# Optimization experiments

Measured on AMD Instinct MI355X. Metric: run time of the kernel, lower is better.

Reference implementation:

```python
import jax, jax.numpy as jnp
import numpy as np

EPS = 1e-12


def sage_pool_conv(x, src, dst, W_pool, b_pool, W_self, W_neigh, b, num_nodes):
    """DGL SAGEConv with aggregator_type='pool':
    h_neigh[v] = max_{u in N(v)} relu(x[u] @ W_pool + b_pool)
    out[v] = x[v] @ W_self + h_neigh[v] @ W_neigh + b
    Zero-in-degree nodes get h_neigh = 0 (DGL fills max over empty set with 0).
    """
    m = jax.nn.relu(x[src] @ W_pool + b_pool)            # [E, F] gathered + transformed
    agg = jax.ops.segment_max(m, dst, num_segments=num_nodes)  # [N, F], -inf where no neighbors
    agg = jnp.where(jnp.isneginf(agg), 0.0, agg)
    return x @ W_self + agg @ W_neigh + b


def l2norm_relu(h):
    # F.normalize(h, p=2, dim=1, eps=1e-12) then relu
    n = jnp.maximum(jnp.linalg.norm(h, axis=1, keepdims=True), EPS)
    return jax.nn.relu(h / n)


def setup_inputs() -> dict:
    key = jax.random.key(0)
    N, E = 50000, 1600000
    IN, HID, OUT = 128, 128, 128
    ks = jax.random.split(key, 16)
    s = 0.05
    return {
        "x": jax.random.normal(ks[0], (N, IN), dtype=jnp.float32),
        "src": jax.random.randint(ks[1], (E,), 0, N, dtype=jnp.int32),
        "dst": jax.random.randint(ks[2], (E,), 0, N, dtype=jnp.int32),
        "W_pool1": jax.random.normal(ks[3], (IN, IN), dtype=jnp.float32) * s,
        "b_pool1": jnp.zeros((IN,), dtype=jnp.float32),
        "W_self1": jax.random.normal(ks[4], (IN, HID), dtype=jnp.float32) * s,
        "W_neigh1": jax.random.normal(ks[5], (IN, HID), dtype=jnp.float32) * s,
        "b1": jnp.zeros((HID,), dtype=jnp.float32),
        "W_pool2": jax.random.normal(ks[6], (HID, HID), dtype=jnp.float32) * s,
        "b_pool2": jnp.zeros((HID,), dtype=jnp.float32),
        "W_self2": jax.random.normal(ks[7], (HID, OUT), dtype=jnp.float32) * s,
        "W_neigh2": jax.random.normal(ks[8], (HID, OUT), dtype=jnp.float32) * s,
        "b2": jnp.zeros((OUT,), dtype=jnp.float32),
    }


def reference(x, src, dst, W_pool1, b_pool1, W_self1, W_neigh1, b1,
              W_pool2, b_pool2, W_self2, W_neigh2, b2):
    N = x.shape[0]
    h = sage_pool_conv(x, src, dst, W_pool1, b_pool1, W_self1, W_neigh1, b1, N)
    h = l2norm_relu(h)
    # dropout_1 is re-assigned in the original forward but never applied -> no dropout
    h = sage_pool_conv(h, src, dst, W_pool2, b_pool2, W_self2, W_neigh2, b2, N)
    h = l2norm_relu(h)
    return h
```

## Files before the change

### kernel.cpp

```cpp
#include <hip/hip_runtime.h>
#include <hip/hip_bf16.h>

#define NF 128

typedef __attribute__((ext_vector_type(8))) short bf8;
typedef __attribute__((ext_vector_type(4))) float f4;
typedef unsigned short u16x8 __attribute__((ext_vector_type(8)));

static __device__ __forceinline__ unsigned short f2bf(float f) {
  unsigned u = __builtin_bit_cast(unsigned, f);
  u = u + 0x7FFF + ((u >> 16) & 1);
  return (unsigned short)(u >> 16);
}

static __device__ __forceinline__ uint4 pkmax4(uint4 a, uint4 b) {
  u16x8 x = __builtin_bit_cast(u16x8, a);
  u16x8 y = __builtin_bit_cast(u16x8, b);
  u16x8 m = __builtin_elementwise_max(x, y);
  return __builtin_bit_cast(uint4, m);
}

static __device__ __forceinline__ uint4 shflxor4(uint4 a, int m) {
  uint4 r;
  r.x = (unsigned)__shfl_xor((int)a.x, m, 64);
  r.y = (unsigned)__shfl_xor((int)a.y, m, 64);
  r.z = (unsigned)__shfl_xor((int)a.z, m, 64);
  r.w = (unsigned)__shfl_xor((int)a.w, m, 64);
  return r;
}


#define TILE_B 8192

__global__ __launch_bounds__(256) void k_prep(
    const float* __restrict__ x, unsigned short* __restrict__ Xb, long long nelX,
    const int* __restrict__ dst, int* __restrict__ bcnt, int E, int gTile,
    const float* W0, const float* W1, const float* W2,
    const float* W3, const float* W4, const float* W5,
    unsigned short* __restrict__ Wpack) {
  __shared__ int h[256];
  int b = blockIdx.x, tid = threadIdx.x;

  long long i = ((long long)b * 256 + tid) * 8;
  if (i + 8 <= nelX) {
    float4 a = *(const float4*)(x + i);
    float4 c = *(const float4*)(x + i + 4);
    uint4 o;
    o.x = f2bf(a.x) | ((unsigned)f2bf(a.y) << 16);
    o.y = f2bf(a.z) | ((unsigned)f2bf(a.w) << 16);
    o.z = f2bf(c.x) | ((unsigned)f2bf(c.y) << 16);
    o.w = f2bf(c.z) | ((unsigned)f2bf(c.w) << 16);
    *(uint4*)(Xb + i) = o;
  }

  if (b < gTile) {
    h[tid] = 0;
    __syncthreads();
    int t0 = b * TILE_B;
    int tend = min(E, t0 + TILE_B);
    for (int k = t0 + tid; k < tend; k += 256) atomicAdd(&h[dst[k] >> 8], 1);
    __syncthreads();
    if (h[tid] > 0) atomicAdd(&bcnt[tid], h[tid]);
  } else if (b < gTile + 48) {
    int gid = (b - gTile) * 256 + tid;
    int m = gid >> 11;
    int u = gid & 2047;
    const float* W = (m == 0) ? W0 : (m == 1) ? W1 : (m == 2) ? W2
                   : (m == 3) ? W3 : (m == 4) ? W4 : W5;
    int l = u & 63, c = u >> 6;
    int kk = c & 3, t = c >> 2;
    int kb = kk * 32 + ((l >> 4) << 3);
    int n = t * 16 + (l & 15);
    unsigned short* o = Wpack + (size_t)m * 2048 * 8 + (size_t)u * 8;
    #pragma unroll
    for (int j = 0; j < 8; ++j) o[j] = f2bf(W[(size_t)(kb + j) * NF + n]);
  }
}


__global__ __launch_bounds__(256) void k_bscan(const int* __restrict__ bcnt,
                                               int* __restrict__ boff,
                                               int* __restrict__ cursors,
                                               int* __restrict__ off,
                                               int nb, int N, int E) {
  __shared__ int sc[256];
  int tid = threadIdx.x;
  int v = (tid < nb) ? bcnt[tid] : 0;
  sc[tid] = v;
  __syncthreads();
  for (int d = 1; d < 256; d <<= 1) {
    int t = (tid >= d) ? sc[tid - d] : 0;
    __syncthreads();
    sc[tid] += t;
    __syncthreads();
  }
  if (tid < nb) {
    boff[tid + 1] = sc[tid];
    cursors[tid] = sc[tid] - v;
  }
  if (tid == 0) { boff[0] = 0; off[N] = E; }
}

__global__ __launch_bounds__(256) void k_binB(const int* __restrict__ src,
                                              const int* __restrict__ dst,
                                              int* __restrict__ cursors,
                                              unsigned* __restrict__ tmp, int E) {
  __shared__ int h[256], sc[256], gb[256], lc[256];
  __shared__ unsigned sorted[TILE_B];
  int tid = threadIdx.x;
  int t0 = blockIdx.x * TILE_B;
  int tcnt = min(E - t0, TILE_B);
  if (tcnt <= 0) return;
  h[tid] = 0;
  __syncthreads();
  for (int i = tid; i < tcnt; i += 256) atomicAdd(&h[dst[t0 + i] >> 8], 1);
  __syncthreads();
  int v = h[tid];
  sc[tid] = v;
  __syncthreads();
  for (int d = 1; d < 256; d <<= 1) {
    int t = (tid >= d) ? sc[tid - d] : 0;
    __syncthreads();
    sc[tid] += t;
    __syncthreads();
  }
  lc[tid] = 0;
  gb[tid] = (v > 0) ? atomicAdd(&cursors[tid], v) : 0;
  __syncthreads();
  for (int i = tid; i < tcnt; i += 256) {
    int d = dst[t0 + i];
    unsigned s = (unsigned)src[t0 + i];
    int b = d >> 8;
    int p = (sc[b] - h[b]) + atomicAdd(&lc[b], 1);
    sorted[p] = ((unsigned)b << 24) | (s << 8) | (unsigned)(d & 255);
  }
  __syncthreads();
  for (int i = tid; i < tcnt; i += 256) {
    unsigned ev = sorted[i];
    int b = ev >> 24;
    tmp[gb[b] + (i - (sc[b] - h[b]))] = ev & 0xFFFFFFu;
  }
}

#define CSR_CAP 15360

__global__ __launch_bounds__(256) void k_binC(const unsigned* __restrict__ tmp,
                                              const int* __restrict__ boff,
                                              int* __restrict__ off,
                                              unsigned short* __restrict__ esrc, int N) {
  __shared__ int lh[256], ls[256], lcur[256];
  __shared__ int csr[CSR_CAP];
  int tid = threadIdx.x;
  int b = blockIdx.x;
  int base = b << 8;
  int beg = boff[b], end = boff[b + 1];
  int cnt = end - beg;
  lh[tid] = 0;
  __syncthreads();
  for (int i = beg + tid; i < end; i += 256) atomicAdd(&lh[tmp[i] & 255], 1);
  __syncthreads();
  int v = lh[tid];
  ls[tid] = v;
  __syncthreads();
  for (int d = 1; d < 256; d <<= 1) {
    int t = (tid >= d) ? ls[tid - d] : 0;
    __syncthreads();
    ls[tid] += t;
    __syncthreads();
  }
  int excl = ls[tid] - v;
  if (base + tid < N) off[base + tid] = beg + excl;
  lcur[tid] = 0;
  __syncthreads();
  if (cnt <= CSR_CAP) {
    for (int i = beg + tid; i < end; i += 256) {
      unsigned e = tmp[i];
      int dl = (int)(e & 255);
      int p = (ls[dl] - lh[dl]) + atomicAdd(&lcur[dl], 1);
      csr[p] = (int)(e >> 8);
    }
    __syncthreads();
    for (int i = tid; i < cnt; i += 256) esrc[beg + i] = (unsigned short)csr[i];
  } else {
    for (int i = beg + tid; i < end; i += 256) {
      unsigned e = tmp[i];
      int dl = (int)(e & 255);
      int p = (ls[dl] - lh[dl]) + atomicAdd(&lcur[dl], 1);
      esrc[beg + p] = (unsigned short)(e >> 8);
    }
  }
}


template <int NMAT, int OUT_MODE>
__global__ __launch_bounds__(512) void k_gemm_p(
    const unsigned short* __restrict__ A0, const unsigned short* __restrict__ P0,
    const unsigned short* __restrict__ A1, const unsigned short* __restrict__ P1,
    const float* __restrict__ bias, void* __restrict__ Cout, int M) {
  constexpr int STG = (OUT_MODE == 2) ? 8192 : 4096;
  __shared__ __align__(16) char smem[NMAT * 32768 + 8 * STG];
  int tid = threadIdx.x, w = tid >> 6, lane = tid & 63;
  int r0 = lane & 15, g = lane >> 4;

  {
    uint4* S = (uint4*)smem;
    const uint4* Pv0 = (const uint4*)P0;
    for (int t = tid; t < 2048; t += 512) S[t] = Pv0[t];
    if (NMAT == 2) {
      const uint4* Pv1 = (const uint4*)P1;
      for (int t = tid; t < 2048; t += 512) S[2048 + t] = Pv1[t];
    }
  }

  float bb[8];
  #pragma unroll
  for (int t = 0; t < 8; ++t) bb[t] = bias[t * 16 + r0];

  __syncthreads();
  const bf8* Wl = (const bf8*)smem;
  char* myst = smem + NMAT * 32768 + w * STG;

  int T = (M + 15) >> 4;
  int stride = gridDim.x * 8;
  for (int t0i = blockIdx.x * 8 + w; t0i < T; t0i += stride) {
    int rowbase = t0i * 16;
    int arow = min(rowbase + r0, M - 1);

    f4 acc[8];
    #pragma unroll
    for (int t = 0; t < 8; ++t) acc[t] = (f4){0.f, 0.f, 0.f, 0.f};

    #pragma unroll
    for (int mat = 0; mat < NMAT; ++mat) {
      const unsigned short* A = (mat == 0) ? A0 : A1;
      const bf8* Ar = (const bf8*)(A + (size_t)arow * NF);
      const bf8* Wm = Wl + mat * 2048;
      #pragma unroll
      for (int kk = 0; kk < 4; ++kk) {
        bf8 a = Ar[kk * 4 + g];
        #pragma unroll
        for (int t = 0; t < 8; ++t)
          acc[t] = __builtin_amdgcn_mfma_f32_16x16x32_bf16(a, Wm[(t * 4 + kk) * 64 + lane], acc[t], 0, 0, 0);
      }
    }

    float val[8][4];
    #pragma unroll
    for (int t = 0; t < 8; ++t)
      #pragma unroll
      for (int i = 0; i < 4; ++i) val[t][i] = acc[t][i] + bb[t];

    float inv[4] = {1.f, 1.f, 1.f, 1.f};
    if (OUT_MODE != 0) {
      float ss[4] = {0.f, 0.f, 0.f, 0.f};
      #pragma unroll
      for (int i = 0; i < 4; ++i)
        #pragma unroll
        for (int t = 0; t < 8; ++t) ss[i] += val[t][i] * val[t][i];
      #pragma unroll
      for (int d = 1; d < 16; d <<= 1)
        #pragma unroll
        for (int i = 0; i < 4; ++i) ss[i] += __shfl_xor(ss[i], d, 64);
      #pragma unroll
      for (int i = 0; i < 4; ++i) inv[i] = 1.f / fmaxf(sqrtf(ss[i]), 1e-12f);
    }

    int maxrows = min(16, M - rowbase);
    if (OUT_MODE == 2) {
      float* So = (float*)myst;
      #pragma unroll
      for (int i = 0; i < 4; ++i)
        #pragma unroll
        for (int t = 0; t < 8; ++t)
          So[(g * 4 + i) * NF + t * 16 + r0] = fmaxf(val[t][i] * inv[i], 0.f);
      uint4* Og = (uint4*)((float*)Cout + (size_t)rowbase * NF);
      const uint4* Sv = (const uint4*)myst;
      int maxc = maxrows * 32;
      #pragma unroll
      for (int k = 0; k < 8; ++k) {
        int c = lane + k * 64;
        if (c < maxc) Og[c] = Sv[c];
      }
    } else {
      unsigned short* So = (unsigned short*)myst;
      #pragma unroll
      for (int i = 0; i < 4; ++i)
        #pragma unroll
        for (int t = 0; t < 8; ++t)
          So[(g * 4 + i) * NF + t * 16 + r0] =
              f2bf(OUT_MODE == 0 ? fmaxf(val[t][i] + 0.f, 0.f) * 1.f
                                 : fmaxf(val[t][i] * inv[i], 0.f));
      uint4* Og = (uint4*)((unsigned short*)Cout + (size_t)rowbase * NF);
      const uint4* Sv = (const uint4*)myst;
      int maxc = maxrows * 16;
      #pragma unroll
      for (int k = 0; k < 4; ++k) {
        int c = lane + k * 64;
        if (c < maxc) Og[c] = Sv[c];
      }
    }
  }
}


__global__ __launch_bounds__(256) void k_gather_max(
    const unsigned short* __restrict__ Y, const int* __restrict__ off,
    const unsigned short* __restrict__ esrc, unsigned short* __restrict__ AGG, int N) {
  int w = (blockIdx.x * 256 + threadIdx.x) >> 6;
  int lane = threadIdx.x & 63;
  if (w >= N) return;
  int r0 = lane & 15, g = lane >> 4;
  int s = __builtin_amdgcn_readfirstlane(off[w]);
  int e = __builtin_amdgcn_readfirstlane(off[w + 1]);
  uint4 am[8];
  #pragma unroll
  for (int j = 0; j < 8; ++j) am[j] = (uint4){0u, 0u, 0u, 0u};
  for (int b0 = s; b0 < e; b0 += 64) {
    int cnt = min(64, e - b0);
    int idxv = (int)esrc[b0 + min(lane, cnt - 1)];
    for (int i = 0; i < cnt; i += 32) {
      uint4 v[8];
      #pragma unroll
      for (int j = 0; j < 8; ++j) {
        int eo = min(i + j * 4 + g, cnt - 1);
        int u = __shfl(idxv, eo, 64);
        v[j] = *((const uint4*)(Y + (size_t)u * NF) + r0);
      }
      #pragma unroll
      for (int j = 0; j < 8; ++j) am[j] = pkmax4(am[j], v[j]);
    }
  }
  am[0] = pkmax4(am[0], am[1]); am[2] = pkmax4(am[2], am[3]);
  am[4] = pkmax4(am[4], am[5]); am[6] = pkmax4(am[6], am[7]);
  am[0] = pkmax4(am[0], am[2]); am[4] = pkmax4(am[4], am[6]);
  uint4 a = pkmax4(am[0], am[4]);
  a = pkmax4(a, shflxor4(a, 16));
  a = pkmax4(a, shflxor4(a, 32));
  if (g == 0) *(uint4*)(AGG + (size_t)w * NF + r0 * 8) = a;
}


extern "C" void kernel_launch(void* const* d_in, const int* in_sizes, int n_in,
                              void* d_out, int out_size, void* d_ws, size_t ws_size,
                              hipStream_t stream) {
  const float* x   = (const float*)d_in[0];
  const int*   src = (const int*)d_in[1];
  const int*   dst = (const int*)d_in[2];
  const float* Wp1 = (const float*)d_in[3];
  const float* bp1 = (const float*)d_in[4];
  const float* Ws1 = (const float*)d_in[5];
  const float* Wn1 = (const float*)d_in[6];
  const float* b1  = (const float*)d_in[7];
  const float* Wp2 = (const float*)d_in[8];
  const float* bp2 = (const float*)d_in[9];
  const float* Ws2 = (const float*)d_in[10];
  const float* Wn2 = (const float*)d_in[11];
  const float* b2  = (const float*)d_in[12];
  float* out = (float*)d_out;

  const int N = in_sizes[0] / NF;
  const int E = in_sizes[1];
  const int NB = (N + 255) >> 8;

  char* ws = (char*)d_ws;
  auto carve = [&](size_t bytes) { char* p = ws; ws += (bytes + 255) & ~(size_t)255; return p; };
  unsigned short* Xb    = (unsigned short*)carve((size_t)N * NF * 2);
  unsigned short* Yb    = (unsigned short*)carve((size_t)N * NF * 2);
  unsigned short* AGGb  = (unsigned short*)carve((size_t)N * NF * 2);
  unsigned short* Hb    = (unsigned short*)carve((size_t)N * NF * 2);
  unsigned short* Wpack = (unsigned short*)carve((size_t)6 * NF * NF * 2);
  int* off     = (int*)carve((size_t)(N + 1) * 4);
  int* bcnt    = (int*)carve((size_t)NB * 4);
  int* boff    = (int*)carve((size_t)(NB + 1) * 4);
  int* cursors = (int*)carve((size_t)NB * 4);
  unsigned* tmp = (unsigned*)carve((size_t)E * 4);
  unsigned short* esrc = (unsigned short*)carve((size_t)E * 2);

  unsigned short* Pp1 = Wpack + 0 * NF * NF;
  unsigned short* Ps1 = Wpack + 1 * NF * NF;
  unsigned short* Pn1 = Wpack + 2 * NF * NF;
  unsigned short* Pp2 = Wpack + 3 * NF * NF;
  unsigned short* Ps2 = Wpack + 4 * NF * NF;
  unsigned short* Pn2 = Wpack + 5 * NF * NF;

  const long long nelX = (long long)N * NF;
  const int gConv = (int)((nelX / 8 + 255) / 256);
  const int gTile = (E + TILE_B - 1) / TILE_B;
  const int gRW   = (N + 3) / 4;

  hipMemsetAsync(bcnt, 0, (size_t)NB * 4, stream);
  k_prep<<<gConv, 256, 0, stream>>>(x, Xb, nelX, dst, bcnt, E, gTile,
                                    Wp1, Ws1, Wn1, Wp2, Ws2, Wn2, Wpack);
  k_bscan<<<1, 256, 0, stream>>>(bcnt, boff, cursors, off, NB, N, E);
  k_binB<<<gTile, 256, 0, stream>>>(src, dst, cursors, tmp, E);
  k_binC<<<NB, 256, 0, stream>>>(tmp, boff, off, esrc, N);

  k_gemm_p<1, 0><<<512, 512, 0, stream>>>(Xb, Pp1, nullptr, nullptr, bp1, Yb, N);
  k_gather_max<<<gRW, 256, 0, stream>>>(Yb, off, esrc, AGGb, N);
  k_gemm_p<2, 1><<<256, 512, 0, stream>>>(Xb, Ps1, AGGb, Pn1, b1, Hb, N);

  k_gemm_p<1, 0><<<512, 512, 0, stream>>>(Hb, Pp2, nullptr, nullptr, bp2, Yb, N);
  k_gather_max<<<gRW, 256, 0, stream>>>(Yb, off, esrc, AGGb, N);
  k_gemm_p<2, 2><<<256, 512, 0, stream>>>(Hb, Ps2, AGGb, Pn2, b2, out, N);
}
```

Before: 300.2 us.

## Drop bucket-scan kernel, slab-sort CSR by source, split GEMMs, shrink gather unroll

Removes the single-block k_bscan launch by having each k_binB and k_binC block recompute the bucket prefix sum from the counts. k_binC now sorts each node's edges into source-index slabs, so gathers within a node walk source rows roughly in ascending order for better cache locality. The dual GEMM becomes a one-tile-per-wave kernel that reads packed weights straight from global memory instead of staging them in LDS. The gather-max loop is reduced from 8 to 4 in-flight loads per lane. These trade redundant scans and less memory-level parallelism for one fewer launch, better locality and higher occupancy.

```diff
diff --git a/kernel.cpp b/kernel.cpp
--- a/kernel.cpp
+++ b/kernel.cpp
@@ -2,6 +2,10 @@
 #include <hip/hip_bf16.h>
 
 #define NF 128
+#define TILE_B 8192
+#define NSLAB 8
+#define SLAB_SHIFT 13
+#define CSR_CAP 15360
 
 typedef __attribute__((ext_vector_type(8))) short bf8;
 typedef __attribute__((ext_vector_type(4))) float f4;
@@ -29,8 +33,6 @@
   return r;
 }
 
-
-#define TILE_B 8192
 
 __global__ __launch_bounds__(256) void k_prep(
     const float* __restrict__ x, unsigned short* __restrict__ Xb, long long nelX,
@@ -78,105 +80,128 @@
 }
 
 
-__global__ __launch_bounds__(256) void k_bscan(const int* __restrict__ bcnt,
-                                               int* __restrict__ boff,
-                                               int* __restrict__ cursors,
-                                               int* __restrict__ off,
-                                               int nb, int N, int E) {
-  __shared__ int sc[256];
-  int tid = threadIdx.x;
-  int v = (tid < nb) ? bcnt[tid] : 0;
-  sc[tid] = v;
-  __syncthreads();
-  for (int d = 1; d < 256; d <<= 1) {
-    int t = (tid >= d) ? sc[tid - d] : 0;
-    __syncthreads();
-    sc[tid] += t;
-    __syncthreads();
-  }
-  if (tid < nb) {
-    boff[tid + 1] = sc[tid];
-    cursors[tid] = sc[tid] - v;
-  }
-  if (tid == 0) { boff[0] = 0; off[N] = E; }
-}
-
 __global__ __launch_bounds__(256) void k_binB(const int* __restrict__ src,
                                               const int* __restrict__ dst,
-                                              int* __restrict__ cursors,
+                                              const int* __restrict__ bcnt,
+                                              int* __restrict__ gcur,
                                               unsigned* __restrict__ tmp, int E) {
-  __shared__ int h[256], sc[256], gb[256], lc[256];
+  __shared__ int h[256], hs[256], gb[256], lc[256], bo[256];
   __shared__ unsigned sorted[TILE_B];
   int tid = threadIdx.x;
   int t0 = blockIdx.x * TILE_B;
   int tcnt = min(E - t0, TILE_B);
   if (tcnt <= 0) return;
+
+  int bv = bcnt[tid];
+  hs[tid] = bv;
+  __syncthreads();
+  for (int d = 1; d < 256; d <<= 1) {
+    int t = (tid >= d) ? hs[tid - d] : 0;
+    __syncthreads();
+    hs[tid] += t;
+    __syncthreads();
+  }
+  bo[tid] = hs[tid] - bv;
   h[tid] = 0;
   __syncthreads();
+
   for (int i = tid; i < tcnt; i += 256) atomicAdd(&h[dst[t0 + i] >> 8], 1);
   __syncthreads();
   int v = h[tid];
-  sc[tid] = v;
+  hs[tid] = v;
   __syncthreads();
   for (int d = 1; d < 256; d <<= 1) {
-    int t = (tid >= d) ? sc[tid - d] : 0;
-    __syncthreads();
-    sc[tid] += t;
+    int t = (tid >= d) ? hs[tid - d] : 0;
+    __syncthreads();
+    hs[tid] += t;
     __syncthreads();
   }
   lc[tid] = 0;
-  gb[tid] = (v > 0) ? atomicAdd(&cursors[tid], v) : 0;
+  gb[tid] = bo[tid] + ((v > 0) ? atomicAdd(&gcur[tid], v) : 0);
   __syncthreads();
   for (int i = tid; i < tcnt; i += 256) {
     int d = dst[t0 + i];
     unsigned s = (unsigned)src[t0 + i];
     int b = d >> 8;
-    int p = (sc[b] - h[b]) + atomicAdd(&lc[b], 1);
+    int p = (hs[b] - h[b]) + atomicAdd(&lc[b], 1);
     sorted[p] = ((unsigned)b << 24) | (s << 8) | (unsigned)(d & 255);
   }
   __syncthreads();
   for (int i = tid; i < tcnt; i += 256) {
     unsigned ev = sorted[i];
     int b = ev >> 24;
-    tmp[gb[b] + (i - (sc[b] - h[b]))] = ev & 0xFFFFFFu;
-  }
-}
-
-#define CSR_CAP 15360
+    tmp[gb[b] + (i - (hs[b] - h[b]))] = ev & 0xFFFFFFu;
+  }
+}
+
 
 __global__ __launch_bounds__(256) void k_binC(const unsigned* __restrict__ tmp,
-                                              const int* __restrict__ boff,
+                                              const int* __restrict__ bcnt,
                                               int* __restrict__ off,
-                                              unsigned short* __restrict__ esrc, int N) {
-  __shared__ int lh[256], ls[256], lcur[256];
+                                              unsigned short* __restrict__ esrc,
+                                              int N, int E) {
+  __shared__ int pre[256 * NSLAB];
+  __shared__ int lc2[256 * NSLAB];
+  __shared__ int s256[256];
+  __shared__ int bo[256];
   __shared__ int csr[CSR_CAP];
   int tid = threadIdx.x;
   int b = blockIdx.x;
   int base = b << 8;
-  int beg = boff[b], end = boff[b + 1];
-  int cnt = end - beg;
-  lh[tid] = 0;
-  __syncthreads();
-  for (int i = beg + tid; i < end; i += 256) atomicAdd(&lh[tmp[i] & 255], 1);
-  __syncthreads();
-  int v = lh[tid];
-  ls[tid] = v;
+
+  int bv = bcnt[tid];
+  s256[tid] = bv;
   __syncthreads();
   for (int d = 1; d < 256; d <<= 1) {
-    int t = (tid >= d) ? ls[tid - d] : 0;
-    __syncthreads();
-    ls[tid] += t;
-    __syncthreads();
-  }
-  int excl = ls[tid] - v;
-  if (base + tid < N) off[base + tid] = beg + excl;
-  lcur[tid] = 0;
-  __syncthreads();
+    int t = (tid >= d) ? s256[tid - d] : 0;
+    __syncthreads();
+    s256[tid] += t;
+    __syncthreads();
+  }
+  bo[tid] = s256[tid] - bv;
+  for (int k = tid; k < 256 * NSLAB; k += 256) { pre[k] = 0; lc2[k] = 0; }
+  __syncthreads();
+
+  int beg = bo[b];
+  int cnt = bcnt[b];
+  int end = beg + cnt;
+
+  for (int i = beg + tid; i < end; i += 256) {
+    unsigned e = tmp[i];
+    int key = ((e & 255) << 3) | (e >> (8 + SLAB_SHIFT));
+    atomicAdd(&pre[key], 1);
+  }
+  __syncthreads();
+  {
+    int sum = 0;
+    #pragma unroll
+    for (int j = 0; j < NSLAB; ++j) {
+      int v = pre[tid * NSLAB + j];
+      pre[tid * NSLAB + j] = sum;
+      sum += v;
+    }
+    s256[tid] = sum;
+    __syncthreads();
+    for (int d = 1; d < 256; d <<= 1) {
+      int t = (tid >= d) ? s256[tid - d] : 0;
+      __syncthreads();
+      s256[tid] += t;
+      __syncthreads();
+    }
+    int segbase = s256[tid] - sum;
+    #pragma unroll
+    for (int j = 0; j < NSLAB; ++j) pre[tid * NSLAB + j] += segbase;
+  }
+  __syncthreads();
+
+  if (base + tid < N) off[base + tid] = beg + pre[tid * NSLAB];
+  if (b == 0 && tid == 0) off[N] = E;
+
   if (cnt <= CSR_CAP) {
     for (int i = beg + tid; i < end; i += 256) {
       unsigned e = tmp[i];
-      int dl = (int)(e & 255);
-      int p = (ls[dl] - lh[dl]) + atomicAdd(&lcur[dl], 1);
+      int key = ((e & 255) << 3) | (e >> (8 + SLAB_SHIFT));
+      int p = pre[key] + atomicAdd(&lc2[key], 1);
       csr[p] = (int)(e >> 8);
     }
     __syncthreads();
@@ -184,41 +209,33 @@
   } else {
     for (int i = beg + tid; i < end; i += 256) {
       unsigned e = tmp[i];
-      int dl = (int)(e & 255);
-      int p = (ls[dl] - lh[dl]) + atomicAdd(&lcur[dl], 1);
+      int key = ((e & 255) << 3) | (e >> (8 + SLAB_SHIFT));
+      int p = pre[key] + atomicAdd(&lc2[key], 1);
       esrc[beg + p] = (unsigned short)(e >> 8);
     }
   }
 }
 
 
-template <int NMAT, int OUT_MODE>
-__global__ __launch_bounds__(512) void k_gemm_p(
-    const unsigned short* __restrict__ A0, const unsigned short* __restrict__ P0,
-    const unsigned short* __restrict__ A1, const unsigned short* __restrict__ P1,
-    const float* __restrict__ bias, void* __restrict__ Cout, int M) {
-  constexpr int STG = (OUT_MODE == 2) ? 8192 : 4096;
-  __shared__ __align__(16) char smem[NMAT * 32768 + 8 * STG];
+__global__ __launch_bounds__(512) void k_gemm_pool(
+    const unsigned short* __restrict__ A, const unsigned short* __restrict__ P,
+    const float* __restrict__ bias, unsigned short* __restrict__ Yout, int M) {
+  __shared__ __align__(16) char smem[32768 + 8 * 4096];
   int tid = threadIdx.x, w = tid >> 6, lane = tid & 63;
   int r0 = lane & 15, g = lane >> 4;
 
   {
     uint4* S = (uint4*)smem;
-    const uint4* Pv0 = (const uint4*)P0;
-    for (int t = tid; t < 2048; t += 512) S[t] = Pv0[t];
-    if (NMAT == 2) {
-      const uint4* Pv1 = (const uint4*)P1;
-      for (int t = tid; t < 2048; t += 512) S[2048 + t] = Pv1[t];
-    }
-  }
-
+    const uint4* Pv = (const uint4*)P;
+    for (int t = tid; t < 2048; t += 512) S[t] = Pv[t];
+  }
   float bb[8];
   #pragma unroll
   for (int t = 0; t < 8; ++t) bb[t] = bias[t * 16 + r0];
-
-  __syncthreads();
+  __syncthreads();
+
   const bf8* Wl = (const bf8*)smem;
-  char* myst = smem + NMAT * 32768 + w * STG;
+  char* myst = smem + 32768 + w * 4096;
 
   int T = (M + 15) >> 4;
   int stride = gridDim.x * 8;
@@ -230,74 +247,118 @@
     #pragma unroll
     for (int t = 0; t < 8; ++t) acc[t] = (f4){0.f, 0.f, 0.f, 0.f};
 
-    #pragma unroll
-    for (int mat = 0; mat < NMAT; ++mat) {
-      const unsigned short* A = (mat == 0) ? A0 : A1;
-      const bf8* Ar = (const bf8*)(A + (size_t)arow * NF);
-      const bf8* Wm = Wl + mat * 2048;
-      #pragma unroll
-      for (int kk = 0; kk < 4; ++kk) {
-        bf8 a = Ar[kk * 4 + g];
-        #pragma unroll
-        for (int t = 0; t < 8; ++t)
-          acc[t] = __builtin_amdgcn_mfma_f32_16x16x32_bf16(a, Wm[(t * 4 + kk) * 64 + lane], acc[t], 0, 0, 0);
-      }
-    }
-
-    float val[8][4];
-    #pragma unroll
-    for (int t = 0; t < 8; ++t)
-      #pragma unroll
-      for (int i = 0; i < 4; ++i) val[t][i] = acc[t][i] + bb[t];
-
-    float inv[4] = {1.f, 1.f, 1.f, 1.f};
-    if (OUT_MODE != 0) {
-      float ss[4] = {0.f, 0.f, 0.f, 0.f};
-      #pragma unroll
-      for (int i = 0; i < 4; ++i)
-        #pragma unroll
-        for (int t = 0; t < 8; ++t) ss[i] += val[t][i] * val[t][i];
-      #pragma unroll
-      for (int d = 1; d < 16; d <<= 1)
-        #pragma unroll
-        for (int i = 0; i < 4; ++i) ss[i] += __shfl_xor(ss[i], d, 64);
-      #pragma unroll
-      for (int i = 0; i < 4; ++i) inv[i] = 1.f / fmaxf(sqrtf(ss[i]), 1e-12f);
-    }
-
-    int maxrows = min(16, M - rowbase);
-    if (OUT_MODE == 2) {
-      float* So = (float*)myst;
-      #pragma unroll
-      for (int i = 0; i < 4; ++i)
-        #pragma unroll
-        for (int t = 0; t < 8; ++t)
-          So[(g * 4 + i) * NF + t * 16 + r0] = fmaxf(val[t][i] * inv[i], 0.f);
-      uint4* Og = (uint4*)((float*)Cout + (size_t)rowbase * NF);
-      const uint4* Sv = (const uint4*)myst;
-      int maxc = maxrows * 32;
-      #pragma unroll
-      for (int k = 0; k < 8; ++k) {
-        int c = lane + k * 64;
-        if (c < maxc) Og[c] = Sv[c];
-      }
-    } else {
-      unsigned short* So = (unsigned short*)myst;
-      #pragma unroll
-      for (int i = 0; i < 4; ++i)
-        #pragma unroll
-        for (int t = 0; t < 8; ++t)
-          So[(g * 4 + i) * NF + t * 16 + r0] =
-              f2bf(OUT_MODE == 0 ? fmaxf(val[t][i] + 0.f, 0.f) * 1.f
-                                 : fmaxf(val[t][i] * inv[i], 0.f));
-      uint4* Og = (uint4*)((unsigned short*)Cout + (size_t)rowbase * NF);
-      const uint4* Sv = (const uint4*)myst;
-      int maxc = maxrows * 16;
-      #pragma unroll
-      for (int k = 0; k < 4; ++k) {
-        int c = lane + k * 64;
-        if (c < maxc) Og[c] = Sv[c];
-      }
+    const bf8* Ar = (const bf8*)(A + (size_t)arow * NF);
+    #pragma unroll
+    for (int kk = 0; kk < 4; ++kk) {
+      bf8 a = Ar[kk * 4 + g];
+      #pragma unroll
+      for (int t = 0; t < 8; ++t)
+        acc[t] = __builtin_amdgcn_mfma_f32_16x16x32_bf16(a, Wl[(t * 4 + kk) * 64 + lane], acc[t], 0, 0, 0);
+    }
+
+    unsigned short* So = (unsigned short*)myst;
+    #pragma unroll
+    for (int i = 0; i < 4; ++i)
+      #pragma unroll
+      for (int t = 0; t < 8; ++t)
+        So[(g * 4 + i) * NF + t * 16 + r0] = f2bf(fmaxf(acc[t][i] + bb[t], 0.f));
+    uint4* Og = (uint4*)(Yout + (size_t)rowbase * NF);
+    const uint4* Sv = (const uint4*)myst;
+    int maxc = min(16, M - rowbase) * 16;
+    #pragma unroll
+    for (int k = 0; k < 4; ++k) {
+      int c = lane + k * 64;
+      if (c < maxc) Og[c] = Sv[c];
+    }
+  }
+}
+
+
+template <int OUT_MODE>
+__global__ __launch_bounds__(256) void k_gemm_dual(
+    const unsigned short* __restrict__ A0, const unsigned short* __restrict__ P0,
+    const unsigned short* __restrict__ A1, const unsigned short* __restrict__ P1,
+    const float* __restrict__ bias, void* __restrict__ Cout, int M) {
+  constexpr int STG = (OUT_MODE == 2) ? 8192 : 4096;
+  __shared__ __align__(16) char smem[4 * STG];
+  int tid = threadIdx.x, w = tid >> 6, lane = tid & 63;
+  int r0 = lane & 15, g = lane >> 4;
+  int rowbase = (blockIdx.x * 4 + w) * 16;
+  if (rowbase >= M) return;
+  int arow = min(rowbase + r0, M - 1);
+  char* myst = smem + w * STG;
+
+  f4 acc[8];
+  #pragma unroll
+  for (int t = 0; t < 8; ++t) acc[t] = (f4){0.f, 0.f, 0.f, 0.f};
+
+  #pragma unroll
+  for (int mat = 0; mat < 2; ++mat) {
+    const unsigned short* A = (mat == 0) ? A0 : A1;
+    const bf8* Pp = (const bf8*)((mat == 0) ? P0 : P1);
+    const bf8* Ar = (const bf8*)(A + (size_t)arow * NF);
+    #pragma unroll
+    for (int kk = 0; kk < 4; ++kk) {
+      bf8 a = Ar[kk * 4 + g];
+      #pragma unroll
+      for (int t = 0; t < 8; ++t)
+        acc[t] = __builtin_amdgcn_mfma_f32_16x16x32_bf16(a, Pp[(t * 4 + kk) * 64 + lane], acc[t], 0, 0, 0);
+    }
+  }
+
+  float bb[8];
+  #pragma unroll
+  for (int t = 0; t < 8; ++t) bb[t] = bias[t * 16 + r0];
+
+  float val[8][4];
+  #pragma unroll
+  for (int t = 0; t < 8; ++t)
+    #pragma unroll
+    for (int i = 0; i < 4; ++i) val[t][i] = acc[t][i] + bb[t];
+
+  float ss[4] = {0.f, 0.f, 0.f, 0.f};
+  #pragma unroll
+  for (int i = 0; i < 4; ++i)
+    #pragma unroll
+    for (int t = 0; t < 8; ++t) ss[i] += val[t][i] * val[t][i];
+  #pragma unroll
+  for (int d = 1; d < 16; d <<= 1)
+    #pragma unroll
+    for (int i = 0; i < 4; ++i) ss[i] += __shfl_xor(ss[i], d, 64);
+  float inv[4];
+  #pragma unroll
+  for (int i = 0; i < 4; ++i) inv[i] = 1.f / fmaxf(sqrtf(ss[i]), 1e-12f);
+
+  int maxrows = min(16, M - rowbase);
+  if (OUT_MODE == 2) {
+    float* So = (float*)myst;
+    #pragma unroll
+    for (int i = 0; i < 4; ++i)
+      #pragma unroll
+      for (int t = 0; t < 8; ++t)
+        So[(g * 4 + i) * NF + t * 16 + r0] = fmaxf(val[t][i] * inv[i], 0.f);
+    uint4* Og = (uint4*)((float*)Cout + (size_t)rowbase * NF);
+    const uint4* Sv = (const uint4*)myst;
+    int maxc = maxrows * 32;
+    #pragma unroll
+    for (int k = 0; k < 8; ++k) {
+      int c = lane + k * 64;
+      if (c < maxc) Og[c] = Sv[c];
+    }
+  } else {
+    unsigned short* So = (unsigned short*)myst;
+    #pragma unroll
+    for (int i = 0; i < 4; ++i)
+      #pragma unroll
+      for (int t = 0; t < 8; ++t)
+        So[(g * 4 + i) * NF + t * 16 + r0] = f2bf(fmaxf(val[t][i] * inv[i], 0.f));
+    uint4* Og = (uint4*)((unsigned short*)Cout + (size_t)rowbase * NF);
+    const uint4* Sv = (const uint4*)myst;
+    int maxc = maxrows * 16;
+    #pragma unroll
+    for (int k = 0; k < 4; ++k) {
+      int c = lane + k * 64;
+      if (c < maxc) Og[c] = Sv[c];
     }
   }
 }
@@ -312,28 +373,25 @@
   int r0 = lane & 15, g = lane >> 4;
   int s = __builtin_amdgcn_readfirstlane(off[w]);
   int e = __builtin_amdgcn_readfirstlane(off[w + 1]);
-  uint4 am[8];
-  #pragma unroll
-  for (int j = 0; j < 8; ++j) am[j] = (uint4){0u, 0u, 0u, 0u};
+  uint4 am[4];
+  #pragma unroll
+  for (int j = 0; j < 4; ++j) am[j] = (uint4){0u, 0u, 0u, 0u};
   for (int b0 = s; b0 < e; b0 += 64) {
     int cnt = min(64, e - b0);
     int idxv = (int)esrc[b0 + min(lane, cnt - 1)];
-    for (int i = 0; i < cnt; i += 32) {
-      uint4 v[8];
-      #pragma unroll
-      for (int j = 0; j < 8; ++j) {
+    for (int i = 0; i < cnt; i += 16) {
+      #pragma unroll
+      for (int j = 0; j < 4; ++j) {
         int eo = min(i + j * 4 + g, cnt - 1);
         int u = __shfl(idxv, eo, 64);
-        v[j] = *((const uint4*)(Y + (size_t)u * NF) + r0);
+        uint4 v = *((const uint4*)(Y + (size_t)u * NF) + r0);
+        am[j] = pkmax4(am[j], v);
       }
-      #pragma unroll
-      for (int j = 0; j < 8; ++j) am[j] = pkmax4(am[j], v[j]);
-    }
-  }
-  am[0] = pkmax4(am[0], am[1]); am[2] = pkmax4(am[2], am[3]);
-  am[4] = pkmax4(am[4], am[5]); am[6] = pkmax4(am[6], am[7]);
-  am[0] = pkmax4(am[0], am[2]); am[4] = pkmax4(am[4], am[6]);
-  uint4 a = pkmax4(am[0], am[4]);
+    }
+  }
+  uint4 a01 = pkmax4(am[0], am[1]);
+  uint4 a23 = pkmax4(am[2], am[3]);
+  uint4 a = pkmax4(a01, a23);
   a = pkmax4(a, shflxor4(a, 16));
   a = pkmax4(a, shflxor4(a, 32));
   if (g == 0) *(uint4*)(AGG + (size_t)w * NF + r0 * 8) = a;
@@ -360,7 +418,6 @@
 
   const int N = in_sizes[0] / NF;
   const int E = in_sizes[1];
-  const int NB = (N + 255) >> 8;
 
   char* ws = (char*)d_ws;
   auto carve = [&](size_t bytes) { char* p = ws; ws += (bytes + 255) & ~(size_t)255; return p; };
@@ -370,11 +427,12 @@
   unsigned short* Hb    = (unsigned short*)carve((size_t)N * NF * 2);
   unsigned short* Wpack = (unsigned short*)carve((size_t)6 * NF * NF * 2);
   int* off     = (int*)carve((size_t)(N + 1) * 4);
-  int* bcnt    = (int*)carve((size_t)NB * 4);
-  int* boff    = (int*)carve((size_t)(NB + 1) * 4);
-  int* cursors = (int*)carve((size_t)NB * 4);
+  int* meta    = (int*)carve(512 * 4);
   unsigned* tmp = (unsigned*)carve((size_t)E * 4);
   unsigned short* esrc = (unsigned short*)carve((size_t)E * 2);
+
+  int* bcnt = meta;
+  int* gcur = meta + 256;
 
   unsigned short* Pp1 = Wpack + 0 * NF * NF;
   unsigned short* Ps1 = Wpack + 1 * NF * NF;
@@ -386,20 +444,21 @@
   const long long nelX = (long long)N * NF;
   const int gConv = (int)((nelX / 8 + 255) / 256);
   const int gTile = (E + TILE_B - 1) / TILE_B;
+  const int NB    = (N + 255) >> 8;
   const int gRW   = (N + 3) / 4;
-
-  hipMemsetAsync(bcnt, 0, (size_t)NB * 4, stream);
+  const int gDual = (((N + 15) >> 4) + 3) / 4;
+
+  hipMemsetAsync(meta, 0, 512 * 4, stream);
   k_prep<<<gConv, 256, 0, stream>>>(x, Xb, nelX, dst, bcnt, E, gTile,
                                     Wp1, Ws1, Wn1, Wp2, Ws2, Wn2, Wpack);
-  k_bscan<<<1, 256, 0, stream>>>(bcnt, boff, cursors, off, NB, N, E);
-  k_binB<<<gTile, 256, 0, stream>>>(src, dst, cursors, tmp, E);
-  k_binC<<<NB, 256, 0, stream>>>(tmp, boff, off, esrc, N);
-
-  k_gemm_p<1, 0><<<512, 512, 0, stream>>>(Xb, Pp1, nullptr, nullptr, bp1, Yb, N);
+  k_binB<<<gTile, 256, 0, stream>>>(src, dst, bcnt, gcur, tmp, E);
+  k_binC<<<NB, 256, 0, stream>>>(tmp, bcnt, off, esrc, N, E);
+
+  k_gemm_pool<<<512, 512, 0, stream>>>(Xb, Pp1, bp1, Yb, N);
   k_gather_max<<<gRW, 256, 0, stream>>>(Yb, off, esrc, AGGb, N);
-  k_gemm_p<2, 1><<<256, 512, 0, stream>>>(Xb, Ps1, AGGb, Pn1, b1, Hb, N);
-
-  k_gemm_p<1, 0><<<512, 512, 0, stream>>>(Hb, Pp2, nullptr, nullptr, bp2, Yb, N);
+  k_gemm_dual<1><<<gDual, 256, 0, stream>>>(Xb, Ps1, AGGb, Pn1, b1, Hb, N);
+
+  k_gemm_pool<<<512, 512, 0, stream>>>(Hb, Pp2, bp2, Yb, N);
   k_gather_max<<<gRW, 256, 0, stream>>>(Yb, off, esrc, AGGb, N);
-  k_gemm_p<2, 2><<<256, 512, 0, stream>>>(Hb, Ps2, AGGb, Pn2, b2, out, N);
-}
+  k_gemm_dual<2><<<gDual, 256, 0, stream>>>(Hb, Ps2, AGGb, Pn2, b2, out, N);
+}
```

Result: slower. 308.6 us (+2.8%).
